# Performance work log

Hardware: AMD Instinct MI355X
Metric: run time of the kernel (lower is better)

## Reference

```python
import jax, jax.numpy as jnp
import numpy as np

_SHAPE = (4, 2, 8, 256, 513)  # N, 2(real/imag), C, T, F


def setup_inputs() -> dict:
    key = jax.random.key(0)
    k1, k2, k3 = jax.random.split(key, 3)
    return {
        "mixture": jax.random.normal(k1, _SHAPE, dtype=jnp.float32),
        "target": jax.random.normal(k2, _SHAPE, dtype=jnp.float32),
        "noise": jax.random.normal(k3, _SHAPE, dtype=jnp.float32),
        "ref_mic_idx": 0,
    }


def _to_complex(x):
    # (N, 2, C, T, F) real-imag stacked -> complex (N, C, T, F)
    return jax.lax.complex(x[:, 0], x[:, 1])


def _mean_spatial_cov(s):
    # s: complex (N, C, T, F) -> time-averaged covariance (N, F, C, C)
    N, C, T, F = s.shape
    sc = jnp.transpose(s, (0, 3, 2, 1))  # (N, F, T, C)
    # outer product V V^H summed over T, fused into one batched GEMM
    return jnp.einsum("nftc,nftd->nfcd", sc, jnp.conj(sc)) / T


def reference(mixture, target, noise, ref_mic_idx):
    y = _to_complex(mixture)  # (N, C, T, F)
    x = _to_complex(target)
    v = _to_complex(noise)
    N, C, T, F = y.shape

    phi_target = _mean_spatial_cov(x)  # (N, F, C, C)
    # diagonal loading: torch adds load to BOTH real and imag parts (RI dim broadcast)
    load = (0.001 / np.sqrt(2)) * (1.0 + 1.0j)
    phi_noise = _mean_spatial_cov(v) + jnp.asarray(load, dtype=y.dtype) * jnp.eye(C, dtype=y.dtype)

    G = jnp.linalg.inv(phi_noise) @ phi_target  # (N, F, C, C)
    l = jnp.trace(G, axis1=-2, axis2=-1)  # (N, F)
    # W = (1/l) * G @ e_ref  -> select column ref_mic_idx
    W = G[..., ref_mic_idx] / l[..., None]  # (N, F, C)

    # X_bf(n,t,f) = W^H y = sum_c conj(W)_{nfc} y_{nctf}
    X_bf = jnp.einsum("nfc,nctf->ntf", jnp.conj(W), y)  # (N, T, F)
    # restack real/imag and add singleton channel dim -> (N, 2, 1, T, F)
    out = jnp.stack([X_bf.real, X_bf.imag], axis=1)[:, :, None]
    return out
```

## Files before the change

### kernel.cpp

```cpp
#include <hip/hip_runtime.h>

#define Nn 4
#define Cc 8
#define Tt 256
#define Ff 513
#define TFs (Tt * Ff)
#define NPAIR 36

template <int G>
__device__ __forceinline__ void cov_body(const float* __restrict__ base,
                                         float* __restrict__ dst,
                                         int t0, int tchunk)
{
    constexpr int R2 = 7 - G;
    float ar[9], ai[9];
#pragma unroll
    for (int s = 0; s < 9; ++s) { ar[s] = 0.f; ai[s] = 0.f; }

    const float* bt = base + (size_t)t0 * Ff;
    for (int tt = 0; tt < tchunk; ++tt) {
        float re[8], im[8];
#pragma unroll
        for (int c = G; c < 8; ++c) {
            re[c] = bt[(size_t)c * TFs];
            im[c] = bt[(size_t)(Cc + c) * TFs];
        }
        int s = 0;
#pragma unroll
        for (int d = G; d < 8; ++d, ++s) {
            ar[s] += re[G] * re[d] + im[G] * im[d];
            ai[s] += im[G] * re[d] - re[G] * im[d];
        }
#pragma unroll
        for (int d = R2; d < 8; ++d, ++s) {
            ar[s] += re[R2] * re[d] + im[R2] * im[d];
            ai[s] += im[R2] * re[d] - re[R2] * im[d];
        }
        bt += Ff;
    }

    int s = 0;
#pragma unroll
    for (int d = G; d < 8; ++d, ++s) {
        const int p = G * 8 - G * (G - 1) / 2 + (d - G);
        dst[(size_t)(p * 2 + 0) * Ff] = ar[s];
        dst[(size_t)(p * 2 + 1) * Ff] = ai[s];
    }
#pragma unroll
    for (int d = R2; d < 8; ++d, ++s) {
        const int p = R2 * 8 - R2 * (R2 - 1) / 2 + (d - R2);
        dst[(size_t)(p * 2 + 0) * Ff] = ar[s];
        dst[(size_t)(p * 2 + 1) * Ff] = ai[s];
    }
}

__global__ __launch_bounds__(64) void cov_partial(
    const float* __restrict__ target, const float* __restrict__ noise,
    float* __restrict__ partial, int nchunk, int tchunk)
{
    int f = blockIdx.x * 64 + threadIdx.x;
    if (f >= Ff) return;
    int n = blockIdx.y;
    int z = blockIdx.z;
    int g = z & 3;
    int inp = (z >> 2) & 1;
    int chunk = z >> 3;

    const float* src = inp ? noise : target;
    const float* base = src + (size_t)n * 2 * Cc * TFs + f;
    float* dst = partial +
        ((((size_t)inp * Nn + n) * nchunk + chunk) * (NPAIR * 2)) * Ff + f;
    int t0 = chunk * tchunk;

    switch (g) {
        case 0: cov_body<0>(base, dst, t0, tchunk); break;
        case 1: cov_body<1>(base, dst, t0, tchunk); break;
        case 2: cov_body<2>(base, dst, t0, tchunk); break;
        default: cov_body<3>(base, dst, t0, tchunk); break;
    }
}

__global__ __launch_bounds__(128) void mvdr_weights(
    const float* __restrict__ partial, const int* __restrict__ ref_ptr,
    float2* __restrict__ wconj, int nchunk)
{
    int f = blockIdx.x;
    int n = blockIdx.y;
    int tid = threadIdx.x;

    __shared__ float covT[72], covN[72];
    __shared__ float2 A[8][16];
    __shared__ float2 PT[8][8];
    __shared__ float2 gcol[8], trp[8];
    __shared__ int piv;

    if (tid < 72) {
        float sT = 0.f, sN = 0.f;
        for (int ch = 0; ch < nchunk; ++ch) {
            size_t iT = ((((size_t)0 * Nn + n) * nchunk + ch) * 72 + tid) * Ff + f;
            size_t iN = ((((size_t)1 * Nn + n) * nchunk + ch) * 72 + tid) * Ff + f;
            sT += partial[iT];
            sN += partial[iN];
        }
        covT[tid] = sT;
        covN[tid] = sN;
    }
    __syncthreads();

    const float invT = 1.0f / (float)Tt;
    const float dl = 0.001f / 1.41421356237309515f;

    if (tid < 64) {
        int r = tid >> 3, c = tid & 7;
        int lo = r <= c ? r : c, hi = r <= c ? c : r;
        int p = lo * 8 - lo * (lo - 1) / 2 + (hi - lo);
        float pr = covN[2 * p] * invT, pi = covN[2 * p + 1] * invT;
        if (r > c) pi = -pi;
        if (r == c) { pr += dl; pi += dl; }
        A[r][c] = make_float2(pr, pi);
        A[r][8 + c] = make_float2(r == c ? 1.f : 0.f, 0.f);
        float qr = covT[2 * p] * invT, qi = covT[2 * p + 1] * invT;
        if (r > c) qi = -qi;
        PT[r][c] = make_float2(qr, qi);
    }
    __syncthreads();

    int r = tid >> 4, col = tid & 15;
    for (int k = 0; k < 8; ++k) {
        if (tid == 0) {
            int best = k;
            float bm = A[k][k].x * A[k][k].x + A[k][k].y * A[k][k].y;
            for (int j = k + 1; j < 8; ++j) {
                float m = A[j][k].x * A[j][k].x + A[j][k].y * A[j][k].y;
                if (m > bm) { bm = m; best = j; }
            }
            piv = best;
        }
        __syncthreads();
        int pv_row = piv;
        if (pv_row != k && tid < 16) {
            float2 tmp = A[k][tid]; A[k][tid] = A[pv_row][tid]; A[pv_row][tid] = tmp;
        }
        __syncthreads();
        if (tid < 16) {
            float2 pv = A[k][k];
            float d = pv.x * pv.x + pv.y * pv.y;
            float2 ip = make_float2(pv.x / d, -pv.y / d);
            float2 a = A[k][tid];
            A[k][tid] = make_float2(a.x * ip.x - a.y * ip.y,
                                    a.x * ip.y + a.y * ip.x);
        }
        __syncthreads();
        float2 factor = A[r][k];
        float2 akc = A[k][col];
        if (r != k) {
            float2 v = A[r][col];
            A[r][col] = make_float2(v.x - (factor.x * akc.x - factor.y * akc.y),
                                    v.y - (factor.x * akc.y + factor.y * akc.x));
        }
        __syncthreads();
    }

    int ref = *ref_ptr;
    if (tid < 8) {
        float2 g = make_float2(0.f, 0.f), tr = make_float2(0.f, 0.f);
#pragma unroll
        for (int d = 0; d < 8; ++d) {
            float2 iv = A[tid][8 + d];
            float2 b = PT[d][ref];
            g.x += iv.x * b.x - iv.y * b.y;
            g.y += iv.x * b.y + iv.y * b.x;
            float2 b2 = PT[d][tid];
            tr.x += iv.x * b2.x - iv.y * b2.y;
            tr.y += iv.x * b2.y + iv.y * b2.x;
        }
        gcol[tid] = g; trp[tid] = tr;
    }
    __syncthreads();
    if (tid < 8) {
        float lx = 0.f, ly = 0.f;
#pragma unroll
        for (int j = 0; j < 8; ++j) { lx += trp[j].x; ly += trp[j].y; }
        float den = lx * lx + ly * ly;
        float2 g = gcol[tid];
        float wx = (g.x * lx + g.y * ly) / den;
        float wy = (g.y * lx - g.x * ly) / den;
        wconj[((size_t)n * Ff + f) * 8 + tid] = make_float2(wx, -wy);
    }
}

__global__ __launch_bounds__(256) void beamform(
    const float* __restrict__ y, const float2* __restrict__ wconj,
    float* __restrict__ out)
{
    int idx = blockIdx.x * 256 + threadIdx.x;
    int n = idx / TFs;
    int rem = idx - n * TFs;
    int t = rem / Ff;
    int f = rem - t * Ff;

    size_t base_re = (size_t)n * 2 * Cc * TFs + (size_t)t * Ff + f;
    size_t base_im = base_re + (size_t)Cc * TFs;
    const float2* w = wconj + ((size_t)n * Ff + f) * 8;

    float xr = 0.f, xi = 0.f;
#pragma unroll
    for (int c = 0; c < Cc; ++c) {
        float yre = y[base_re + (size_t)c * TFs];
        float yim = y[base_im + (size_t)c * TFs];
        float2 wc = w[c];
        xr += wc.x * yre - wc.y * yim;
        xi += wc.x * yim + wc.y * yre;
    }
    size_t ob = (size_t)n * 2 * TFs + (size_t)t * Ff + f;
    out[ob] = xr;
    out[ob + TFs] = xi;
}

extern "C" void kernel_launch(void* const* d_in, const int* in_sizes, int n_in,
                              void* d_out, int out_size, void* d_ws, size_t ws_size,
                              hipStream_t stream) {
    const float* mixture = (const float*)d_in[0];
    const float* target  = (const float*)d_in[1];
    const float* noise   = (const float*)d_in[2];
    const int*   refp    = (const int*)d_in[3];
    float* out = (float*)d_out;

    const size_t wconj_bytes = (size_t)Nn * Ff * 8 * sizeof(float2);
    int nchunk = 8;
    while (nchunk > 1 &&
           (size_t)2 * Nn * nchunk * 72 * Ff * sizeof(float) + wconj_bytes > ws_size)
        nchunk >>= 1;
    int tchunk = Tt / nchunk;

    float*  partial = (float*)d_ws;
    float2* wconj = (float2*)((char*)d_ws +
                              (size_t)2 * Nn * nchunk * 72 * Ff * sizeof(float));

    cov_partial<<<dim3(9, Nn, nchunk * 8), 64, 0, stream>>>(
        target, noise, partial, nchunk, tchunk);
    mvdr_weights<<<dim3(Ff, Nn), 128, 0, stream>>>(partial, refp, wconj, nchunk);
    beamform<<<dim3((Nn * TFs) / 256), 256, 0, stream>>>(mixture, wconj, out);
}
```

Baseline: 161.3 us.

## Solve MVDR systems in registers with wave shuffles, four bins per block

The per-frequency weight kernel now runs four frequency problems per 64-thread wave. Each of 16 lanes holds one column of the augmented matrix [Phi_noise | Phi_target] in registers. Gauss-Jordan elimination uses __shfl for pivot selection and row factors instead of shared memory and about 32 __syncthreads per problem. Solving against Phi_target directly yields inv(N)·T, so the separate inverse-times-matrix product is dropped and the trace comes from a shuffle reduction. The costs are higher register pressure and a changed partial-sum read pattern, which now groups 4 adjacent frequencies per load.

After: 173.3 us. 7.4% more time.

```diff
diff --git a/kernel.cpp b/kernel.cpp
--- a/kernel.cpp
+++ b/kernel.cpp
@@ -80,112 +80,121 @@
     }
 }
 
-__global__ __launch_bounds__(128) void mvdr_weights(
+__global__ __launch_bounds__(64) void mvdr_weights(
     const float* __restrict__ partial, const int* __restrict__ ref_ptr,
     float2* __restrict__ wconj, int nchunk)
 {
-    int f = blockIdx.x;
-    int n = blockIdx.y;
-    int tid = threadIdx.x;
-
-    __shared__ float covT[72], covN[72];
-    __shared__ float2 A[8][16];
-    __shared__ float2 PT[8][8];
-    __shared__ float2 gcol[8], trp[8];
-    __shared__ int piv;
-
-    if (tid < 72) {
-        float sT = 0.f, sN = 0.f;
-        for (int ch = 0; ch < nchunk; ++ch) {
-            size_t iT = ((((size_t)0 * Nn + n) * nchunk + ch) * 72 + tid) * Ff + f;
-            size_t iN = ((((size_t)1 * Nn + n) * nchunk + ch) * 72 + tid) * Ff + f;
-            sT += partial[iT];
-            sN += partial[iN];
-        }
-        covT[tid] = sT;
-        covN[tid] = sN;
+    const int lane = threadIdx.x;
+    const int n = blockIdx.y;
+    const int fbase = blockIdx.x * 4;
+
+    __shared__ float cov[4][144];
+
+    {
+        int prob = lane & 3;
+        int j = lane >> 2;
+        int f = fbase + prob;
+#pragma unroll
+        for (int s = 0; s < 9; ++s) {
+            int v = j * 9 + s;
+            int inp = v >= 72;
+            int p = inp ? v - 72 : v;
+            float acc = 0.f;
+            if (f < Ff) {
+                for (int ch = 0; ch < nchunk; ++ch) {
+                    size_t idx = ((((size_t)inp * Nn + n) * nchunk + ch) * 72 + p)
+                                 * Ff + f;
+                    acc += partial[idx];
+                }
+            }
+            cov[prob][v] = acc;
+        }
     }
     __syncthreads();
+
+    const int prob = lane >> 4;
+    const int col = lane & 15;
+    const int f = fbase + prob;
 
     const float invT = 1.0f / (float)Tt;
     const float dl = 0.001f / 1.41421356237309515f;
 
-    if (tid < 64) {
-        int r = tid >> 3, c = tid & 7;
-        int lo = r <= c ? r : c, hi = r <= c ? c : r;
-        int p = lo * 8 - lo * (lo - 1) / 2 + (hi - lo);
-        float pr = covN[2 * p] * invT, pi = covN[2 * p + 1] * invT;
-        if (r > c) pi = -pi;
-        if (r == c) { pr += dl; pi += dl; }
-        A[r][c] = make_float2(pr, pi);
-        A[r][8 + c] = make_float2(r == c ? 1.f : 0.f, 0.f);
-        float qr = covT[2 * p] * invT, qi = covT[2 * p + 1] * invT;
-        if (r > c) qi = -qi;
-        PT[r][c] = make_float2(qr, qi);
-    }
-    __syncthreads();
-
-    int r = tid >> 4, col = tid & 15;
+    float Ar[8], Ai[8];
+    {
+        const bool left = (col < 8);
+        const int c = left ? col : col - 8;
+        const float* cv = &cov[prob][left ? 72 : 0];
+#pragma unroll
+        for (int r = 0; r < 8; ++r) {
+            int lo = r <= c ? r : c, hi = r <= c ? c : r;
+            int p = lo * 8 - lo * (lo - 1) / 2 + (hi - lo);
+            float vr = cv[2 * p] * invT;
+            float vi = cv[2 * p + 1] * invT;
+            if (r > c) vi = -vi;
+            if (left && r == c) { vr += dl; vi += dl; }
+            Ar[r] = vr; Ai[r] = vi;
+        }
+    }
+
+#pragma unroll
     for (int k = 0; k < 8; ++k) {
-        if (tid == 0) {
-            int best = k;
-            float bm = A[k][k].x * A[k][k].x + A[k][k].y * A[k][k].y;
-            for (int j = k + 1; j < 8; ++j) {
-                float m = A[j][k].x * A[j][k].x + A[j][k].y * A[j][k].y;
+        int best = k;
+        float bm = Ar[k] * Ar[k] + Ai[k] * Ai[k];
+#pragma unroll
+        for (int j = 0; j < 8; ++j) {
+            if (j > k) {
+                float m = Ar[j] * Ar[j] + Ai[j] * Ai[j];
                 if (m > bm) { bm = m; best = j; }
             }
-            piv = best;
-        }
-        __syncthreads();
-        int pv_row = piv;
-        if (pv_row != k && tid < 16) {
-            float2 tmp = A[k][tid]; A[k][tid] = A[pv_row][tid]; A[pv_row][tid] = tmp;
-        }
-        __syncthreads();
-        if (tid < 16) {
-            float2 pv = A[k][k];
-            float d = pv.x * pv.x + pv.y * pv.y;
-            float2 ip = make_float2(pv.x / d, -pv.y / d);
-            float2 a = A[k][tid];
-            A[k][tid] = make_float2(a.x * ip.x - a.y * ip.y,
-                                    a.x * ip.y + a.y * ip.x);
-        }
-        __syncthreads();
-        float2 factor = A[r][k];
-        float2 akc = A[k][col];
-        if (r != k) {
-            float2 v = A[r][col];
-            A[r][col] = make_float2(v.x - (factor.x * akc.x - factor.y * akc.y),
-                                    v.y - (factor.x * akc.y + factor.y * akc.x));
-        }
-        __syncthreads();
+        }
+        int bk = __shfl(best, k, 16);
+
+        float tr = Ar[k], ti = Ai[k];
+#pragma unroll
+        for (int j = 0; j < 8; ++j) {
+            if (j == bk && j != k) {
+                Ar[k] = Ar[j]; Ai[k] = Ai[j];
+                Ar[j] = tr;    Ai[j] = ti;
+            }
+        }
+
+        float pr = __shfl(Ar[k], k, 16);
+        float pi = __shfl(Ai[k], k, 16);
+        float d = pr * pr + pi * pi;
+        float ir = pr / d, ii = -pi / d;
+        float nr = Ar[k] * ir - Ai[k] * ii;
+        float ni = Ar[k] * ii + Ai[k] * ir;
+        Ar[k] = nr; Ai[k] = ni;
+
+#pragma unroll
+        for (int r = 0; r < 8; ++r) {
+            float fr = __shfl(Ar[r], k, 16);
+            float fi = __shfl(Ai[r], k, 16);
+            if (r != k) {
+                Ar[r] -= fr * Ar[k] - fi * Ai[k];
+                Ai[r] -= fr * Ai[k] + fi * Ar[k];
+            }
+        }
+    }
+
+    float tlr = 0.f, tli = 0.f;
+    if (col >= 8) { tlr = Ar[col - 8]; tli = Ai[col - 8]; }
+#pragma unroll
+    for (int off = 1; off < 16; off <<= 1) {
+        tlr += __shfl_xor(tlr, off, 16);
+        tli += __shfl_xor(tli, off, 16);
     }
 
     int ref = *ref_ptr;
-    if (tid < 8) {
-        float2 g = make_float2(0.f, 0.f), tr = make_float2(0.f, 0.f);
-#pragma unroll
-        for (int d = 0; d < 8; ++d) {
-            float2 iv = A[tid][8 + d];
-            float2 b = PT[d][ref];
-            g.x += iv.x * b.x - iv.y * b.y;
-            g.y += iv.x * b.y + iv.y * b.x;
-            float2 b2 = PT[d][tid];
-            tr.x += iv.x * b2.x - iv.y * b2.y;
-            tr.y += iv.x * b2.y + iv.y * b2.x;
-        }
-        gcol[tid] = g; trp[tid] = tr;
-    }
-    __syncthreads();
-    if (tid < 8) {
-        float lx = 0.f, ly = 0.f;
-#pragma unroll
-        for (int j = 0; j < 8; ++j) { lx += trp[j].x; ly += trp[j].y; }
-        float den = lx * lx + ly * ly;
-        float2 g = gcol[tid];
-        float wx = (g.x * lx + g.y * ly) / den;
-        float wy = (g.y * lx - g.x * ly) / den;
-        wconj[((size_t)n * Ff + f) * 8 + tid] = make_float2(wx, -wy);
+    if (col == 8 + ref && f < Ff) {
+        float den = tlr * tlr + tli * tli;
+        float2* wp = wconj + ((size_t)n * Ff + f) * 8;
+#pragma unroll
+        for (int r = 0; r < 8; ++r) {
+            float wx = (Ar[r] * tlr + Ai[r] * tli) / den;
+            float wy = (Ai[r] * tlr - Ar[r] * tli) / den;
+            wp[r] = make_float2(wx, -wy);
+        }
     }
 }
 
@@ -239,6 +248,7 @@
 
     cov_partial<<<dim3(9, Nn, nchunk * 8), 64, 0, stream>>>(
         target, noise, partial, nchunk, tchunk);
-    mvdr_weights<<<dim3(Ff, Nn), 128, 0, stream>>>(partial, refp, wconj, nchunk);
+    mvdr_weights<<<dim3((Ff + 3) / 4, Nn), 64, 0, stream>>>(
+        partial, refp, wconj, nchunk);
     beamform<<<dim3((Nn * TFs) / 256), 256, 0, stream>>>(mixture, wconj, out);
 }
```
